# Performance work log

Hardware: AMD Instinct MI355X
Metric: run time of the kernel (lower is better)

Reference implementation:

```python
import jax, jax.numpy as jnp
import numpy as np

B, N, DIM, H, DH = 8, 1024, 768, 12, 64  # batch, seq, d_model, heads, dim_head
INNER = H * DH


def setup_inputs() -> dict:
    key = jax.random.key(0)
    ks = jax.random.split(key, 6)
    s = 1.0 / np.sqrt(DIM)
    return {
        "x": jax.random.normal(ks[0], (B, N, DIM), dtype=jnp.float32),
        "Wq": jax.random.normal(ks[1], (DIM, INNER), dtype=jnp.float32) * s,
        "Wkv": jax.random.normal(ks[2], (DIM, 2 * INNER), dtype=jnp.float32) * s,
        "mix_pre": jax.random.normal(ks[3], (H, H), dtype=jnp.float32) * (1.0 / H),
        "mix_post": jax.random.normal(ks[4], (H, H), dtype=jnp.float32) * (1.0 / H),
        "Wo": jax.random.normal(ks[5], (INNER, DIM), dtype=jnp.float32) * s,
        "bo": jnp.zeros((DIM,), dtype=jnp.float32),
    }


def reference(x, Wq, Wkv, mix_pre, mix_post, Wo, bo):
    scale = DH ** -0.5
    q = x @ Wq                                   # [B,N,INNER]
    kv = x @ Wkv                                 # [B,N,2*INNER]
    k, v = jnp.split(kv, 2, axis=-1)
    split_heads = lambda t: t.reshape(B, N, H, DH).transpose(0, 2, 1, 3)  # [B,H,N,DH]
    q, k, v = split_heads(q), split_heads(k), split_heads(v)
    dots = jnp.einsum('bhid,bhjd->bhij', q, k) * scale
    dots = jnp.einsum('bhij,hg->bgij', dots, mix_pre)      # talking-heads pre-softmax
    attn = jax.nn.softmax(dots, axis=-1)
    attn = jnp.einsum('bhij,hg->bgij', attn, mix_post)     # talking-heads post-softmax
    o = jnp.einsum('bhij,bhjd->bhid', attn, v)             # [B,H,N,DH]
    o = o.transpose(0, 2, 1, 3).reshape(B, N, INNER)
    return o @ Wo + bo
```

## Files before the change

### kernel.cpp

```cpp
#include <hip/hip_runtime.h>
#include <cstdint>
#include <cstddef>

typedef unsigned short u16;
typedef unsigned int u32;

typedef __bf16 bf16x8 __attribute__((ext_vector_type(8)));
typedef float f32x4 __attribute__((ext_vector_type(4)));
typedef u32 u32x4 __attribute__((ext_vector_type(4)));
typedef u32 u32x2 __attribute__((ext_vector_type(2)));

#if defined(__has_builtin)
#if __has_builtin(__builtin_amdgcn_global_load_lds)
#define USE_GLL 1
#endif
#endif

typedef const __attribute__((address_space(1))) u32 gas_u32;
typedef __attribute__((address_space(3))) u32 las_u32;

__device__ inline float bf2f(u16 u) {
    union { u32 i; float f; } c; c.i = ((u32)u) << 16; return c.f;
}
__device__ inline u16 f2bf(float f) {
    union { float f; u32 i; } c; c.f = f;
    u32 u = c.i;
    return (u16)((u + 0x7fffu + ((u >> 16) & 1u)) >> 16);
}
__device__ inline f32x4 mfma16(u32x4 a, u32x4 b, f32x4 c) {
    return __builtin_amdgcn_mfma_f32_16x16x32_bf16(
        __builtin_bit_cast(bf16x8, a), __builtin_bit_cast(bf16x8, b), c, 0, 0, 0);
}
__device__ inline u32x4 cvt8(const float* p) {
    f32x4 a = *(const f32x4*)p, b = *(const f32x4*)(p + 4);
    u32x4 v;
    v[0] = (u32)f2bf(a[0]) | ((u32)f2bf(a[1]) << 16);
    v[1] = (u32)f2bf(a[2]) | ((u32)f2bf(a[3]) << 16);
    v[2] = (u32)f2bf(b[0]) | ((u32)f2bf(b[1]) << 16);
    v[3] = (u32)f2bf(b[2]) | ((u32)f2bf(b[3]) << 16);
    return v;
}

__global__ __launch_bounds__(64) void k_detect(const u16* __restrict__ x, u32* __restrict__ flag)
{
    const int lane = threadIdx.x;
    int cnt = 0;
#pragma unroll
    for (int i = 0; i < 4; i++) {
        u32 e = (x[lane * 4 + i] >> 7) & 0xFF;
        cnt += (e >= 115 && e <= 133) ? 1 : 0;
    }
#pragma unroll
    for (int off = 1; off < 64; off <<= 1) cnt += __shfl_xor(cnt, off);
    if (lane == 0) *flag = (cnt >= 192) ? 1u : 0u;
}

__global__ __launch_bounds__(256) void k_convert_x(
    const void* __restrict__ X, u16* __restrict__ xb, const u32* __restrict__ flag)
{
    const bool isb = (*flag != 0);
    const size_t i = ((size_t)blockIdx.x * 256 + threadIdx.x) * 8;
    if (isb) *(u32x4*)(xb + i) = *(const u32x4*)((const u16*)X + i);
    else     *(u32x4*)(xb + i) = cvt8((const float*)X + i);
}

__global__ __launch_bounds__(256) void k_transpose_w(
    const void* __restrict__ Wq, const void* __restrict__ Wkv, const void* __restrict__ Wo,
    u16* __restrict__ WT, u16* __restrict__ WoT, const u32* __restrict__ flag)
{
    const bool isb = (*flag != 0);
    __shared__ __align__(16) u16 t[64][72];
    const int z = blockIdx.z;
    const void* src; u16* dst; int C;
    if (z == 0)      { src = Wq;  dst = WT;             C = 768;  }
    else if (z == 1) { src = Wkv; dst = WT + 768 * 768; C = 1536; }
    else             { src = Wo;  dst = WoT;            C = 768;  }
    const int c0 = blockIdx.y * 64;
    if (c0 >= C) return;
    const int k0 = blockIdx.x * 64;
    const int tid = threadIdx.x;
    const int r = tid >> 3, cc = (tid & 7) * 8;
    if (isb) {
        const u16* s = (const u16*)src;
        for (int rr = r; rr < 64; rr += 32)
            *(u32x4*)&t[rr][cc] = *(const u32x4*)(s + (size_t)(k0 + rr) * C + c0 + cc);
    } else {
        const float* s = (const float*)src;
        for (int rr = r; rr < 64; rr += 32)
            *(u32x4*)&t[rr][cc] = cvt8(s + (size_t)(k0 + rr) * C + c0 + cc);
    }
    __syncthreads();
    const int kk = (tid & 7) * 8;
    for (int ccc = tid >> 3; ccc < 64; ccc += 32) {
        __align__(16) u16 tmp[8];
#pragma unroll
        for (int s = 0; s < 8; s++) tmp[s] = t[kk + s][ccc];
        *(u32x4*)(dst + (size_t)(c0 + ccc) * 768 + k0 + kk) = *(u32x4*)tmp;
    }
}

__global__ __launch_bounds__(256) void k_transpose_v(
    const u16* __restrict__ v, u16* __restrict__ vt)
{
    __shared__ __align__(16) u16 t[64][72];
    const int bh = blockIdx.z;
    const int t0 = blockIdx.x * 64;
    const int tid = threadIdx.x;
    const int r = tid >> 3, cc = (tid & 7) * 8;
    for (int rr = r; rr < 64; rr += 32)
        *(u32x4*)&t[rr][cc] = *(const u32x4*)(v + ((size_t)bh * 1024 + t0 + rr) * 64 + cc);
    __syncthreads();
    const int kk = (tid & 7) * 8;
    for (int ccc = tid >> 3; ccc < 64; ccc += 32) {
        __align__(16) u16 tmp[8];
#pragma unroll
        for (int s = 0; s < 8; s++) tmp[s] = t[kk + s][ccc];
        *(u32x4*)(vt + ((size_t)bh * 64 + ccc) * 1024 + t0 + kk) = *(u32x4*)tmp;
    }
}

__device__ inline void stage_tile(const u16* __restrict__ gA, const u16* __restrict__ gB,
                                  u16* As, u16* Bs, int w, int lane)
{
    const int sr = lane >> 2, sc = (lane & 3) * 8;
#pragma unroll
    for (int i = 0; i < 2; i++) {
        const int rA = w * 16 + i * 64;
        const u16* ga = gA + (size_t)(rA + sr) * 768 + sc;
        const u16* gb = gB + (size_t)(rA + sr) * 768 + sc;
#ifdef USE_GLL
        __builtin_amdgcn_global_load_lds((gas_u32*)ga, (las_u32*)&As[rA * 32], 16, 0, 0);
        __builtin_amdgcn_global_load_lds((gas_u32*)gb, (las_u32*)&Bs[rA * 32], 16, 0, 0);
#else
        *(u32x4*)&As[(rA + sr) * 32 + sc] = *(const u32x4*)ga;
        *(u32x4*)&Bs[(rA + sr) * 32 + sc] = *(const u32x4*)gb;
#endif
    }
}

__global__ __launch_bounds__(256) void k_gemm_qkv(
    const u16* __restrict__ Xb, const u16* __restrict__ WT,
    u16* __restrict__ qb, u16* __restrict__ kb, u16* __restrict__ vb)
{
    __shared__ __align__(16) u16 As[128 * 32];
    __shared__ __align__(16) u16 Bs[128 * 32];
    const int tid = threadIdx.x;
    const int w = tid >> 6, lane = tid & 63, quad = lane >> 4, l15 = lane & 15;
    const int wr = w >> 1, wc = w & 1;
    const int m0 = blockIdx.y * 128, c0 = blockIdx.x * 128;
    f32x4 acc[4][4];
#pragma unroll
    for (int i = 0; i < 4; i++)
#pragma unroll
        for (int j = 0; j < 4; j++) acc[i][j] = (f32x4){0.f, 0.f, 0.f, 0.f};

    for (int k0 = 0; k0 < 768; k0 += 32) {
        __syncthreads();
        stage_tile(Xb + (size_t)m0 * 768 + k0, WT + (size_t)c0 * 768 + k0, As, Bs, w, lane);
        __syncthreads();
        u32x4 af[4], bfv[4];
#pragma unroll
        for (int mi = 0; mi < 4; mi++)
            af[mi] = *(const u32x4*)&As[(wr * 64 + mi * 16 + l15) * 32 + quad * 8];
#pragma unroll
        for (int ni = 0; ni < 4; ni++)
            bfv[ni] = *(const u32x4*)&Bs[(wc * 64 + ni * 16 + l15) * 32 + quad * 8];
#pragma unroll
        for (int mi = 0; mi < 4; mi++)
#pragma unroll
            for (int ni = 0; ni < 4; ni++)
                acc[mi][ni] = mfma16(af[mi], bfv[ni], acc[mi][ni]);
    }
#pragma unroll
    for (int mi = 0; mi < 4; mi++)
#pragma unroll
        for (int ni = 0; ni < 4; ni++) {
            const int c = c0 + wc * 64 + ni * 16 + l15;
            const int sector = c / 768, hc = c % 768;
            const int h = hc >> 6, d = hc & 63;
            u16* dst = sector == 0 ? qb : (sector == 1 ? kb : vb);
#pragma unroll
            for (int r = 0; r < 4; r++) {
                const int tok = m0 + wr * 64 + mi * 16 + quad * 4 + r;
                const int b = tok >> 10, n = tok & 1023;
                dst[(((size_t)b * 12 + h) * 1024 + n) * 64 + d] = f2bf(acc[mi][ni][r]);
            }
        }
}

__global__ __launch_bounds__(256) void k_gemm_out(
    const u16* __restrict__ O, const u16* __restrict__ WoT, const void* __restrict__ bo,
    float* __restrict__ out, const u32* __restrict__ flag)
{
    const bool isb = (*flag != 0);
    __shared__ __align__(16) u16 As[128 * 32];
    __shared__ __align__(16) u16 Bs[128 * 32];
    const int tid = threadIdx.x;
    const int w = tid >> 6, lane = tid & 63, quad = lane >> 4, l15 = lane & 15;
    const int wr = w >> 1, wc = w & 1;
    const int m0 = blockIdx.y * 128, c0 = blockIdx.x * 128;
    f32x4 acc[4][4];
#pragma unroll
    for (int i = 0; i < 4; i++)
#pragma unroll
        for (int j = 0; j < 4; j++) acc[i][j] = (f32x4){0.f, 0.f, 0.f, 0.f};

    for (int k0 = 0; k0 < 768; k0 += 32) {
        __syncthreads();
        stage_tile(O + (size_t)m0 * 768 + k0, WoT + (size_t)c0 * 768 + k0, As, Bs, w, lane);
        __syncthreads();
        u32x4 af[4], bfv[4];
#pragma unroll
        for (int mi = 0; mi < 4; mi++)
            af[mi] = *(const u32x4*)&As[(wr * 64 + mi * 16 + l15) * 32 + quad * 8];
#pragma unroll
        for (int ni = 0; ni < 4; ni++)
            bfv[ni] = *(const u32x4*)&Bs[(wc * 64 + ni * 16 + l15) * 32 + quad * 8];
#pragma unroll
        for (int mi = 0; mi < 4; mi++)
#pragma unroll
            for (int ni = 0; ni < 4; ni++)
                acc[mi][ni] = mfma16(af[mi], bfv[ni], acc[mi][ni]);
    }
#pragma unroll
    for (int mi = 0; mi < 4; mi++)
#pragma unroll
        for (int ni = 0; ni < 4; ni++) {
            const int c = c0 + wc * 64 + ni * 16 + l15;
            const float biasv = isb ? bf2f(((const u16*)bo)[c]) : ((const float*)bo)[c];
#pragma unroll
            for (int r = 0; r < 4; r++) {
                const int tok = m0 + wr * 64 + mi * 16 + quad * 4 + r;
                out[(size_t)tok * 768 + c] = acc[mi][ni][r] + biasv;
            }
        }
}

__global__ __launch_bounds__(768) void k_attn(
    const u16* __restrict__ qb, const u16* __restrict__ kb, const u16* __restrict__ vt,
    const void* __restrict__ mixpre, const void* __restrict__ mixpost,
    u16* __restrict__ ob, u16* __restrict__ E, const u32* __restrict__ flag, int tiles)
{
    __shared__ __align__(16) u16 LDSU[18432];
    __shared__ float invlT[256];
    u16* SP   = LDSU;
    u32* SP32 = (u32*)LDSU;
    u16* Abuf = LDSU;
    float* red = (float*)LDSU;

    const bool isb = (*flag != 0);
    const int tid = threadIdx.x;
    const int w = tid >> 6, lane = tid & 63, quad = lane >> 4, l15 = lane & 15;
    const int bid = blockIdx.x;
    const int b = bid & 7;
    const int nq = gridDim.x >> 3;
    u16* Ewg = E + (size_t)bid * (16384 * 12);

    u32x4 apre = (u32x4){0, 0, 0, 0};
    float mpostF[8];
#pragma unroll
    for (int j = 0; j < 8; j++) {
        const int h = quad * 8 + j;
        mpostF[j] = 0.f;
        if (quad < 2 && l15 < 12 && h < 12) {
            mpostF[j] = isb ? bf2f(((const u16*)mixpost)[h * 12 + l15])
                            : ((const float*)mixpost)[h * 12 + l15];
            u16 v1 = isb ? ((const u16*)mixpre)[h * 12 + l15]
                         : f2bf(((const float*)mixpre)[h * 12 + l15]);
            apre[j >> 1] |= ((u32)v1) << ((j & 1) * 16);
        }
    }

    const u16* kh = kb + ((size_t)b * 12 + w) * 1024 * 64;
    const u16* vh = vt + ((size_t)b * 12 + w) * 64 * 1024;

    for (int tt = 0; tt < tiles; tt++) {
        const int qx = (bid >> 3) + tt * nq;
        const int i0 = qx * 16;

        for (int n = tid; n < 1024; n += 768) { SP32[n * 9 + 6] = 0; SP32[n * 9 + 7] = 0; }

        const u16* qh = qb + (((size_t)b * 12 + w) * 1024 + i0) * 64;
        u32x4 aq[2];
#pragma unroll
        for (int kc = 0; kc < 2; kc++)
            aq[kc] = *(const u32x4*)(qh + l15 * 64 + kc * 32 + quad * 8);

        f32x4 part[6];
#pragma unroll
        for (int t = 0; t < 6; t++) part[t] = (f32x4){0.f, 0.f, 0.f, 0.f};

        for (int jt = 0; jt < 16; jt++) {
            const int j0 = jt * 64;
            f32x4 sc[4];
#pragma unroll
            for (int nt = 0; nt < 4; nt++) {
                f32x4 a = (f32x4){0.f, 0.f, 0.f, 0.f};
#pragma unroll
                for (int kc = 0; kc < 2; kc++) {
                    u32x4 bfr = *(const u32x4*)(kh + (size_t)(j0 + nt * 16 + l15) * 64 + kc * 32 + quad * 8);
                    a = mfma16(aq[kc], bfr, a);
                }
                sc[nt] = a;
            }
            __syncthreads();
#pragma unroll
            for (int nt = 0; nt < 4; nt++)
#pragma unroll
                for (int r = 0; r < 4; r++)
                    SP[((quad * 4 + r) * 64 + nt * 16 + l15) * 18 + w] = f2bf(sc[nt][r] * 0.125f);
            __syncthreads();
#pragma unroll
            for (int t = 0; t < 6; t++) {
                const int s = w + 12 * t;
                if (s < 64) {
                    const int row = s * 16 + l15;
                    u32x4 bfr = (u32x4){0, 0, 0, 0};
                    if (quad < 2) {
                        const u32* p = SP32 + row * 9 + quad * 4;
                        bfr[0] = p[0]; bfr[1] = p[1]; bfr[2] = p[2]; bfr[3] = p[3];
                    }
                    f32x4 d = mfma16(apre, bfr, (f32x4){0.f, 0.f, 0.f, 0.f});
                    const float e0 = __expf(d[0]), e1 = __expf(d[1]);
                    const float e2 = __expf(d[2]), e3 = __expf(d[3]);
                    part[t][0] += e0; part[t][1] += e1;
                    part[t][2] += e2; part[t][3] += e3;
                    if (quad < 3) {
                        u32x2 pk;
                        pk[0] = (u32)f2bf(e0) | ((u32)f2bf(e1) << 16);
                        pk[1] = (u32)f2bf(e2) | ((u32)f2bf(e3) << 16);
                        *(u32x2*)(Ewg + ((size_t)jt * 1024 + row) * 12 + quad * 4) = pk;
                    }
                }
            }
        }
        __syncthreads();
#pragma unroll
        for (int t = 0; t < 6; t++) {
            const int s = w + 12 * t;
            if (s < 64) {
#pragma unroll
                for (int r = 0; r < 4; r++) {
                    float v = part[t][r];
#pragma unroll
                    for (int off = 1; off < 16; off <<= 1) v += __shfl_xor(v, off);
                    if (l15 == 0) red[(((s >> 2) * 16) + quad * 4 + r) * 4 + (s & 3)] = v;
                }
            }
        }
        __syncthreads();
        if (tid < 256) {
            const int h = tid & 15;
            float v = 0.f;
            if (h < 12) {
                const float* q = &red[tid * 4];
                v = 1.f / (q[0] + q[1] + q[2] + q[3]);
            }
            invlT[tid] = v;
        }
        __syncthreads();

        u32x4 Afr[6];
#pragma unroll
        for (int t = 0; t < 6; t++) {
            const int s = w + 12 * t;
            Afr[t] = (u32x4){0, 0, 0, 0};
            if (s < 64 && quad < 2) {
                const int i = s >> 2;
#pragma unroll
                for (int j = 0; j < 8; j++) {
                    const u16 v = f2bf(mpostF[j] * invlT[i * 16 + quad * 8 + j]);
                    Afr[t][j >> 1] |= ((u32)v) << ((j & 1) * 16);
                }
            }
        }

        f32x4 oacc[4];
#pragma unroll
        for (int nt = 0; nt < 4; nt++) oacc[nt] = (f32x4){0.f, 0.f, 0.f, 0.f};

        for (int jt = 0; jt < 16; jt++) {
            const int j0 = jt * 64;
#pragma unroll
            for (int t = 0; t < 6; t++) {
                const int s = w + 12 * t;
                if (s < 64) {
                    const int row = s * 16 + l15, i = s >> 2, jq = s & 3;
                    u32x4 ef = (u32x4){0, 0, 0, 0};
                    if (quad < 2) {
                        const u16* ep = Ewg + ((size_t)jt * 1024 + row) * 12 + quad * 8;
                        u32x2 lo = *(const u32x2*)ep;
                        u32x2 hi = *(const u32x2*)(ep + 4);
                        ef[0] = lo[0]; ef[1] = lo[1]; ef[2] = hi[0]; ef[3] = hi[1];
                    }
                    f32x4 am = mfma16(Afr[t], ef, (f32x4){0.f, 0.f, 0.f, 0.f});
#pragma unroll
                    for (int r = 0; r < 4; r++) {
                        const int g2 = quad * 4 + r;
                        if (g2 < 12)
                            Abuf[g2 * 1160 + i * 72 + jq * 16 + l15] = f2bf(am[r]);
                    }
                }
            }
            __syncthreads();
#pragma unroll
            for (int kc = 0; kc < 2; kc++) {
                u32x4 af = *(const u32x4*)&Abuf[w * 1160 + l15 * 72 + kc * 32 + quad * 8];
#pragma unroll
                for (int nt = 0; nt < 4; nt++) {
                    u32x4 vf = *(const u32x4*)(vh + (size_t)(nt * 16 + l15) * 1024 + j0 + kc * 32 + quad * 8);
                    oacc[nt] = mfma16(af, vf, oacc[nt]);
                }
            }
            __syncthreads();
        }
#pragma unroll
        for (int nt = 0; nt < 4; nt++)
#pragma unroll
            for (int r = 0; r < 4; r++)
                ob[((size_t)b * 1024 + i0 + quad * 4 + r) * 768 + w * 64 + nt * 16 + l15] =
                    f2bf(oacc[nt][r]);
    }
}

extern "C" void kernel_launch(void* const* d_in, const int* in_sizes, int n_in,
                              void* d_out, int out_size, void* d_ws, size_t ws_size,
                              hipStream_t stream)
{
    float* out = (float*)d_out;

    u32* flag = (u32*)d_ws;
    u16* WoT  = (u16*)d_ws + 128;
    u16* qb   = WoT + 768 * 768;
    u16* kb   = qb  + 6291456;
    u16* vtb  = kb  + 6291456;
    u16* obuf = vtb + 6291456;
    u16* vb   = obuf;
    u16* ez   = obuf + 6291456;
    u16* WT   = ez;
    u16* xb   = ez + 2304 * 768;
    u16* E    = ez;

    const size_t base   = 256 + 2ull * (768 * 768 + 4ull * 6291456);
    const size_t eslot  = 16384ull * 12 * 2;
    const size_t need1  = base + 512ull * eslot + 64;
    const size_t need2  = base + 256ull * eslot + 64;

    k_detect     <<<dim3(1), 64,  0, stream>>>((const u16*)d_in[0], flag);
    k_transpose_w<<<dim3(12, 24, 3), 256, 0, stream>>>(d_in[1], d_in[2], d_in[5], WT, WoT, flag);
    k_convert_x  <<<dim3(3072),      256, 0, stream>>>(d_in[0], xb, flag);
    k_gemm_qkv   <<<dim3(18, 64),    256, 0, stream>>>(xb, WT, qb, kb, vb);
    k_transpose_v<<<dim3(16, 1, 96), 256, 0, stream>>>(vb, vtb);
    if (ws_size >= need1)
        k_attn   <<<dim3(512), 768, 0, stream>>>(qb, kb, vtb, d_in[3], d_in[4], obuf, E, flag, 1);
    else
        k_attn   <<<dim3(256), 768, 0, stream>>>(qb, kb, vtb, d_in[3], d_in[4], obuf, E, flag, 2);
    k_gemm_out   <<<dim3(6, 64),     256, 0, stream>>>(obuf, WoT, d_in[6], out, flag);
}
```

Baseline: 466.2 us.

## Double-buffer attention E slabs into LDS and relax barriers to LDS-only waits

The PV phase of the attention kernel now prefetches the next 64-column slab of exponentiated scores (E) into a double-buffered LDS region with async global-to-LDS loads. It reads the current slab from LDS instead of issuing scattered 8-byte global loads. Several __syncthreads are replaced by a barrier that waits only on LDS counters, so outstanding global loads are not drained at each barrier. This costs about 48 KB of extra LDS. Cross-wave visibility of the async-loaded slab depends on per-wave vmcnt waits with no block barrier afterwards, so a race is possible.

```diff
diff --git a/kernel.cpp b/kernel.cpp
--- a/kernel.cpp
+++ b/kernel.cpp
@@ -39,6 +39,12 @@
     v[2] = (u32)f2bf(b[0]) | ((u32)f2bf(b[1]) << 16);
     v[3] = (u32)f2bf(b[2]) | ((u32)f2bf(b[3]) << 16);
     return v;
+}
+
+__device__ inline void bar_lds() {
+    asm volatile("s_waitcnt lgkmcnt(0)" ::: "memory");
+    __builtin_amdgcn_s_barrier();
+    __builtin_amdgcn_sched_barrier(0);
 }
 
 __global__ __launch_bounds__(64) void k_detect(const u16* __restrict__ x, u32* __restrict__ flag)
@@ -236,6 +242,19 @@
         }
 }
 
+__device__ inline void stage_e(const u16* __restrict__ src, u16* dst, int w, int lane)
+{
+#pragma unroll
+    for (int c = 0; c < 2; c++) {
+        const int off = ((w * 2 + c) * 64 + lane) * 8;
+#ifdef USE_GLL
+        __builtin_amdgcn_global_load_lds((gas_u32*)(src + off), (las_u32*)(dst + off), 16, 0, 0);
+#else
+        *(u32x4*)(dst + off) = *(const u32x4*)(src + off);
+#endif
+    }
+}
+
 __global__ __launch_bounds__(768) void k_attn(
     const u16* __restrict__ qb, const u16* __restrict__ kb, const u16* __restrict__ vt,
     const void* __restrict__ mixpre, const void* __restrict__ mixpost,
@@ -243,6 +262,7 @@
 {
     __shared__ __align__(16) u16 LDSU[18432];
     __shared__ float invlT[256];
+    __shared__ __align__(16) u16 Eslab[2][12296];
     u16* SP   = LDSU;
     u32* SP32 = (u32*)LDSU;
     u16* Abuf = LDSU;
@@ -303,13 +323,13 @@
                 }
                 sc[nt] = a;
             }
-            __syncthreads();
+            bar_lds();
 #pragma unroll
             for (int nt = 0; nt < 4; nt++)
 #pragma unroll
                 for (int r = 0; r < 4; r++)
                     SP[((quad * 4 + r) * 64 + nt * 16 + l15) * 18 + w] = f2bf(sc[nt][r] * 0.125f);
-            __syncthreads();
+            bar_lds();
 #pragma unroll
             for (int t = 0; t < 6; t++) {
                 const int s = w + 12 * t;
@@ -360,6 +380,8 @@
         }
         __syncthreads();
 
+        stage_e(Ewg, Eslab[0], w, lane);
+
         u32x4 Afr[6];
 #pragma unroll
         for (int t = 0; t < 6; t++) {
@@ -374,13 +396,22 @@
                 }
             }
         }
+        __syncthreads();
 
         f32x4 oacc[4];
 #pragma unroll
         for (int nt = 0; nt < 4; nt++) oacc[nt] = (f32x4){0.f, 0.f, 0.f, 0.f};
 
         for (int jt = 0; jt < 16; jt++) {
+            const int cur = jt & 1;
             const int j0 = jt * 64;
+            if (jt < 15) {
+                stage_e(Ewg + (size_t)(jt + 1) * 12288, Eslab[cur ^ 1], w, lane);
+                asm volatile("s_waitcnt vmcnt(2)" ::: "memory");
+            } else {
+                asm volatile("s_waitcnt vmcnt(0)" ::: "memory");
+            }
+            __builtin_amdgcn_sched_barrier(0);
 #pragma unroll
             for (int t = 0; t < 6; t++) {
                 const int s = w + 12 * t;
@@ -388,7 +419,7 @@
                     const int row = s * 16 + l15, i = s >> 2, jq = s & 3;
                     u32x4 ef = (u32x4){0, 0, 0, 0};
                     if (quad < 2) {
-                        const u16* ep = Ewg + ((size_t)jt * 1024 + row) * 12 + quad * 8;
+                        const u16* ep = &Eslab[cur][row * 12 + quad * 8];
                         u32x2 lo = *(const u32x2*)ep;
                         u32x2 hi = *(const u32x2*)(ep + 4);
                         ef[0] = lo[0]; ef[1] = lo[1]; ef[2] = hi[0]; ef[3] = hi[1];
@@ -402,7 +433,7 @@
                     }
                 }
             }
-            __syncthreads();
+            bar_lds();
 #pragma unroll
             for (int kc = 0; kc < 2; kc++) {
                 u32x4 af = *(const u32x4*)&Abuf[w * 1160 + l15 * 72 + kc * 32 + quad * 8];
@@ -412,7 +443,7 @@
                     oacc[nt] = mfma16(af, vf, oacc[nt]);
                 }
             }
-            __syncthreads();
+            bar_lds();
         }
 #pragma unroll
         for (int nt = 0; nt < 4; nt++)
```

New measurement: 447.8 us. 3.9% less time.
